# Kernel optimization log

Measured on AMD Instinct MI355X. Metric: run time of the kernel, lower is better.

The kernel has to match this reference:

```python
import jax, jax.numpy as jnp
import numpy as np

N = 20000
F_IN = 128
HID = 128
HEADS = 8
NCLS = 18
NEG_SLOPE = 0.2


def setup_inputs() -> dict:
    key = jax.random.key(0)
    ks = jax.random.split(key, 12)
    x = jax.random.normal(ks[0], (N, F_IN), dtype=jnp.float32)
    edge_index = jax.random.randint(ks[1], (2, 200000), 0, N)
    sc1 = 1.0 / np.sqrt(F_IN)
    sc2 = 1.0 / np.sqrt(HEADS * HID)
    W1 = jax.random.normal(ks[2], (F_IN, HEADS * HID), dtype=jnp.float32) * sc1
    a1_src = jax.random.normal(ks[3], (HEADS, HID), dtype=jnp.float32) * sc1
    a1_dst = jax.random.normal(ks[4], (HEADS, HID), dtype=jnp.float32) * sc1
    b1 = jnp.zeros((HEADS * HID,), dtype=jnp.float32)
    W2 = jax.random.normal(ks[5], (HEADS * HID, NCLS), dtype=jnp.float32) * sc2
    a2_src = jax.random.normal(ks[6], (1, NCLS), dtype=jnp.float32) * sc2
    a2_dst = jax.random.normal(ks[7], (1, NCLS), dtype=jnp.float32) * sc2
    b2 = jnp.zeros((NCLS,), dtype=jnp.float32)
    return {"x": x, "edge_index": edge_index, "W1": W1, "a1_src": a1_src,
            "a1_dst": a1_dst, "b1": b1, "W2": W2, "a2_src": a2_src,
            "a2_dst": a2_dst, "b2": b2}


def gat_conv(x, src, dst, W, a_src, a_dst, b, heads, out_ch):
    n = x.shape[0]
    h = (x @ W).reshape(n, heads, out_ch)              # [N,H,C]
    alpha_s = jnp.sum(h * a_src, axis=-1)              # [N,H]
    alpha_d = jnp.sum(h * a_dst, axis=-1)              # [N,H]
    e = jax.nn.leaky_relu(alpha_s[src] + alpha_d[dst], NEG_SLOPE)  # [E,H]
    # per-destination softmax (segment softmax)
    m = jax.ops.segment_max(e, dst, num_segments=n)
    e = jnp.exp(e - m[dst])
    z = jax.ops.segment_sum(e, dst, num_segments=n)
    alpha = e / (z[dst] + 1e-16)                       # [E,H]
    out = jax.ops.segment_sum(alpha[:, :, None] * h[src], dst, num_segments=n)
    return out.reshape(n, heads * out_ch) + b


def reference(x, edge_index, W1, a1_src, a1_dst, b1, W2, a2_src, a2_dst, b2):
    n = x.shape[0]
    # PyG GATConv adds self-loops by default
    loops = jnp.arange(n, dtype=edge_index.dtype)
    src = jnp.concatenate([edge_index[0], loops])
    dst = jnp.concatenate([edge_index[1], loops])
    h = gat_conv(x, src, dst, W1, a1_src, a1_dst, b1, HEADS, HID)
    h = jax.nn.relu(h)
    # F.dropout(training=self.training) is identity in eval mode
    out = gat_conv(h, src, dst, W2, a2_src, a2_dst, b2, 1, NCLS)
    return out
```

## Files before the change

kernel.cpp:

```cpp
#include <hip/hip_runtime.h>
#include <math.h>

#define FIN 128
#define NH 8
#define HC 128
#define HD (NH*HC)
#define NC 18
#define NW2 32
#define NEG 0.2f

typedef __attribute__((ext_vector_type(8))) short bf16x8;
typedef __attribute__((ext_vector_type(4))) float f32x4;

__device__ __forceinline__ float lrelu(float v){ return v > 0.f ? v : NEG*v; }

__device__ __forceinline__ unsigned short f2b(float f){
  unsigned u = __float_as_uint(f);
  unsigned r = (u + 0x7fffu + ((u >> 16) & 1u)) >> 16;
  return (unsigned short)r;
}
__device__ __forceinline__ float b2f_lo(unsigned u){ return __uint_as_float(u << 16); }
__device__ __forceinline__ float b2f_hi(unsigned u){ return __uint_as_float(u & 0xffff0000u); }

__device__ __forceinline__ void acc8(float* a, float w, uint4 r){
  a[0] += w*b2f_lo(r.x); a[1] += w*b2f_hi(r.x);
  a[2] += w*b2f_lo(r.y); a[3] += w*b2f_hi(r.y);
  a[4] += w*b2f_lo(r.z); a[5] += w*b2f_hi(r.z);
  a[6] += w*b2f_lo(r.w); a[7] += w*b2f_hi(r.w);
}

__global__ __launch_bounds__(1024) void scan_k(const int* __restrict__ deg, int N,
                                               int* __restrict__ off, int* __restrict__ cursor){
  __shared__ int wsum[16];
  int t = threadIdx.x, lane = t & 63, wid = t >> 6;
  int PER = (N + 1023) >> 10;
  int base = t * PER;
  int sum = 0;
  for (int i = 0; i < PER; ++i) {
    int idx = base + i;
    if (idx < N) sum += deg[idx];
  }
  int x = sum;
  #pragma unroll
  for (int o = 1; o < 64; o <<= 1) {
    int y = __shfl_up(x, o, 64);
    if (lane >= o) x += y;
  }
  if (lane == 63) wsum[wid] = x;
  __syncthreads();
  if (wid == 0 && lane < 16) {
    int wv = wsum[lane];
    #pragma unroll
    for (int o = 1; o < 16; o <<= 1) {
      int y = __shfl_up(wv, o, 16);
      if (lane >= o) wv += y;
    }
    wsum[lane] = wv;
  }
  __syncthreads();
  int carry = x - sum + (wid > 0 ? wsum[wid-1] : 0);
  int run = carry;
  for (int i = 0; i < PER; ++i) {
    int idx = base + i;
    if (idx < N) {
      off[idx] = run; cursor[idx] = run;
      run += deg[idx];
    }
  }
  if (base < N && base + PER >= N) off[N] = run;
}

__global__ void scatter_k(const int* __restrict__ ei, int E0, int N,
                          int* __restrict__ cursor, int* __restrict__ csr){
  int e = blockIdx.x*256 + threadIdx.x;
  int tot = E0 + N;
  if (e >= tot) return;
  int src, dst;
  if (e < E0) { src = ei[e]; dst = ei[E0 + e]; }
  else        { src = e - E0; dst = src; }
  int p = atomicAdd(&cursor[dst], 1);
  csr[p] = src;
}

__global__ __launch_bounds__(256) void prep_k(const float* __restrict__ x,
    const float* __restrict__ W1, const float* __restrict__ W2,
    const int* __restrict__ ei,
    unsigned short* __restrict__ xb, unsigned short* __restrict__ w1t,
    unsigned short* __restrict__ w2t, int* __restrict__ deg,
    int total8, int bX, int E0, int N){
  __shared__ unsigned short sT[FIN][64+2];
  int b = blockIdx.x, t = threadIdx.x;
  if (b < bX) {
    int i = b*256 + t;
    if (i < total8) {
      const float4* p = (const float4*)x + (size_t)i*2;
      float4 a = p[0], c = p[1];
      uint4 o;
      o.x = (unsigned)f2b(a.x) | ((unsigned)f2b(a.y) << 16);
      o.y = (unsigned)f2b(a.z) | ((unsigned)f2b(a.w) << 16);
      o.z = (unsigned)f2b(c.x) | ((unsigned)f2b(c.y) << 16);
      o.w = (unsigned)f2b(c.z) | ((unsigned)f2b(c.w) << 16);
      ((uint4*)xb)[i] = o;
    }
    return;
  }
  b -= bX;
  if (b < 16) {
    int n0 = b * 64;
    #pragma unroll
    for (int i = 0; i < 32; ++i) {
      int idx = i*256 + t;
      int k = idx >> 6, nl = idx & 63;
      sT[k][nl] = f2b(W1[(size_t)k*HD + n0 + nl]);
    }
    __syncthreads();
    #pragma unroll
    for (int i = 0; i < 16; ++i) {
      int nl = i*4 + (t >> 6);
      int kp = t & 63;
      unsigned u = (unsigned)sT[2*kp][nl] | ((unsigned)sT[2*kp+1][nl] << 16);
      *(unsigned*)&w1t[(size_t)(n0+nl)*FIN + 2*kp] = u;
    }
    return;
  }
  b -= 16;
  if (b < (NW2*HD)/256) {
    int idx = b*256 + t;
    int n = idx >> 10, k = idx & 1023;
    w2t[idx] = (n < NC) ? f2b(W2[(size_t)k*NC + n]) : (unsigned short)0;
    return;
  }
  b -= (NW2*HD)/256;
  {
    int e = b*256 + t;
    int tot = E0 + N;
    if (e >= tot) return;
    int dst = (e < E0) ? ei[E0 + e] : (e - E0);
    atomicAdd(&deg[dst], 1);
  }
}

__global__ __launch_bounds__(256) void gemm1_mfma_k(const unsigned short* __restrict__ xb,
    const unsigned short* __restrict__ w1t,
    const float* __restrict__ a1s, const float* __restrict__ a1d,
    unsigned short* __restrict__ g1b, float* __restrict__ as1, float* __restrict__ ad1,
    int N){
  __shared__ unsigned short sA[128][136];
  __shared__ unsigned short sB[128][136];
  __shared__ float sAs[2][128], sAd[2][128];
  int t = threadIdx.x, lane = t & 63, wid = t >> 6;
  int bm = blockIdx.x * 128;
  int head = blockIdx.y;
  int bn = head * 128;
  #pragma unroll
  for (int i = 0; i < 2; ++i) {
    int idx = i*256 + t;
    int row = idx >> 2, seg = idx & 3;
    int gm = bm + row;
    uint4 a0,a1,a2,a3;
    if (gm < N) {
      const uint4* gp = (const uint4*)(xb + (size_t)gm*FIN + seg*32);
      a0 = gp[0]; a1 = gp[1]; a2 = gp[2]; a3 = gp[3];
    } else {
      a0 = a1 = a2 = a3 = make_uint4(0,0,0,0);
    }
    uint4* lp = (uint4*)&sA[row][seg*32];
    lp[0]=a0; lp[1]=a1; lp[2]=a2; lp[3]=a3;
  }
  #pragma unroll
  for (int i = 0; i < 2; ++i) {
    int idx = i*256 + t;
    int row = idx >> 2, seg = idx & 3;
    const uint4* gp = (const uint4*)(w1t + (size_t)(bn + row)*FIN + seg*32);
    uint4* lp = (uint4*)&sB[row][seg*32];
    lp[0]=gp[0]; lp[1]=gp[1]; lp[2]=gp[2]; lp[3]=gp[3];
  }
  __syncthreads();
  int wr = wid >> 1, wc = wid & 1;
  int lr = lane & 15, kb = lane >> 4;
  f32x4 acc[4][4];
  #pragma unroll
  for (int mi = 0; mi < 4; ++mi)
    #pragma unroll
    for (int ni = 0; ni < 4; ++ni) {
      f32x4 z = {0.f, 0.f, 0.f, 0.f};
      acc[mi][ni] = z;
    }
  #pragma unroll
  for (int ks = 0; ks < 4; ++ks) {
    int ko = ks*32 + kb*8;
    bf16x8 a[4], b[4];
    #pragma unroll
    for (int mi = 0; mi < 4; ++mi)
      a[mi] = *(const bf16x8*)&sA[wr*64 + mi*16 + lr][ko];
    #pragma unroll
    for (int ni = 0; ni < 4; ++ni)
      b[ni] = *(const bf16x8*)&sB[wc*64 + ni*16 + lr][ko];
    #pragma unroll
    for (int mi = 0; mi < 4; ++mi)
      #pragma unroll
      for (int ni = 0; ni < 4; ++ni)
        acc[mi][ni] = __builtin_amdgcn_mfma_f32_16x16x32_bf16(a[mi], b[ni], acc[mi][ni], 0, 0, 0);
  }
  __syncthreads();

  float a1sv[4], a1dv[4];
  #pragma unroll
  for (int ni = 0; ni < 4; ++ni) {
    int c = wc*64 + ni*16 + lr;
    a1sv[ni] = a1s[head*HC + c];
    a1dv[ni] = a1d[head*HC + c];
  }
  #pragma unroll
  for (int mi = 0; mi < 4; ++mi) {
    #pragma unroll
    for (int r = 0; r < 4; ++r) {
      float ps = acc[mi][0][r]*a1sv[0] + acc[mi][1][r]*a1sv[1]
               + acc[mi][2][r]*a1sv[2] + acc[mi][3][r]*a1sv[3];
      float pd = acc[mi][0][r]*a1dv[0] + acc[mi][1][r]*a1dv[1]
               + acc[mi][2][r]*a1dv[2] + acc[mi][3][r]*a1dv[3];
      #pragma unroll
      for (int o = 1; o < 16; o <<= 1) {
        ps += __shfl_xor(ps, o, 64);
        pd += __shfl_xor(pd, o, 64);
      }
      if (lr == 0) {
        int row = wr*64 + mi*16 + kb*4 + r;
        sAs[wc][row] = ps;
        sAd[wc][row] = pd;
      }
    }
  }
  #pragma unroll
  for (int mi = 0; mi < 4; ++mi)
    #pragma unroll
    for (int ni = 0; ni < 4; ++ni) {
      int col = wc*64 + ni*16 + lr;
      #pragma unroll
      for (int r = 0; r < 4; ++r)
        sA[wr*64 + mi*16 + kb*4 + r][col] = f2b(acc[mi][ni][r]);
    }
  __syncthreads();
  {
    int row = t >> 1, half = t & 1;
    int grow = bm + row;
    if (grow < N) {
      uint4* dst = (uint4*)(g1b + (size_t)grow*HD + bn + half*64);
      const uint4* src = (const uint4*)&sA[row][half*64];
      #pragma unroll
      for (int q = 0; q < 8; ++q) dst[q] = src[q];
    }
    if (t < 128 && bm + t < N) {
      as1[(size_t)(bm + t)*NH + head] = sAs[0][t] + sAs[1][t];
      ad1[(size_t)(bm + t)*NH + head] = sAd[0][t] + sAd[1][t];
    }
  }
}

__global__ __launch_bounds__(256) void attn1_k(const unsigned short* __restrict__ g1b,
    const float* __restrict__ as1, const float* __restrict__ ad1,
    const int* __restrict__ off, const int* __restrict__ csr,
    const float* __restrict__ b1, unsigned short* __restrict__ hb, int N){
  int t = threadIdx.x, lane = t & 63, wid = t >> 6;
  int d = blockIdx.x*4 + wid;
  if (d >= N) return;
  int beg = off[d], deg = off[d+1] - beg;
  int hg = lane >> 3;
  float adg = ad1[d*NH + hg];
  float m = -1e30f, z = 0.f;
  float acc[16];
  #pragma unroll
  for (int i = 0; i < 16; ++i) acc[i] = 0.f;

  int j = 0;
  for (; j + 4 <= deg; j += 4) {
    int s0 = csr[beg+j+0], s1 = csr[beg+j+1], s2 = csr[beg+j+2], s3 = csr[beg+j+3];
    const uint4* p0 = (const uint4*)(g1b + (size_t)s0*HD) + lane*2;
    const uint4* p1 = (const uint4*)(g1b + (size_t)s1*HD) + lane*2;
    const uint4* p2 = (const uint4*)(g1b + (size_t)s2*HD) + lane*2;
    const uint4* p3 = (const uint4*)(g1b + (size_t)s3*HD) + lane*2;
    uint4 r00 = p0[0], r01 = p0[1];
    uint4 r10 = p1[0], r11 = p1[1];
    uint4 r20 = p2[0], r21 = p2[1];
    uint4 r30 = p3[0], r31 = p3[1];
    float e0 = lrelu(as1[s0*NH+hg] + adg);
    float e1 = lrelu(as1[s1*NH+hg] + adg);
    float e2 = lrelu(as1[s2*NH+hg] + adg);
    float e3 = lrelu(as1[s3*NH+hg] + adg);
    float em = fmaxf(fmaxf(e0,e1), fmaxf(e2,e3));
    if (em > m) {
      float sc = __expf(m - em);
      z *= sc;
      #pragma unroll
      for (int i = 0; i < 16; ++i) acc[i] *= sc;
      m = em;
    }
    float w0 = __expf(e0 - m), w1 = __expf(e1 - m);
    float w2 = __expf(e2 - m), w3 = __expf(e3 - m);
    z += w0 + w1 + w2 + w3;
    acc8(acc, w0, r00); acc8(acc+8, w0, r01);
    acc8(acc, w1, r10); acc8(acc+8, w1, r11);
    acc8(acc, w2, r20); acc8(acc+8, w2, r21);
    acc8(acc, w3, r30); acc8(acc+8, w3, r31);
  }
  for (; j < deg; ++j) {
    int s = csr[beg+j];
    const uint4* p = (const uint4*)(g1b + (size_t)s*HD) + lane*2;
    uint4 r0 = p[0], r1 = p[1];
    float e = lrelu(as1[s*NH+hg] + adg);
    if (e > m) {
      float sc = __expf(m - e);
      z *= sc;
      #pragma unroll
      for (int i = 0; i < 16; ++i) acc[i] *= sc;
      m = e;
    }
    float w = __expf(e - m);
    z += w;
    acc8(acc, w, r0); acc8(acc+8, w, r1);
  }

  float zinv = 1.f / (z + 1e-16f);
  int cb = lane*16;
  uint o[8];
  #pragma unroll
  for (int q = 0; q < 4; ++q) {
    float4 bv = *(const float4*)&b1[cb + q*4];
    float v0 = fmaxf(acc[q*4+0]*zinv + bv.x, 0.f);
    float v1 = fmaxf(acc[q*4+1]*zinv + bv.y, 0.f);
    float v2 = fmaxf(acc[q*4+2]*zinv + bv.z, 0.f);
    float v3 = fmaxf(acc[q*4+3]*zinv + bv.w, 0.f);
    o[q*2+0] = (unsigned)f2b(v0) | ((unsigned)f2b(v1) << 16);
    o[q*2+1] = (unsigned)f2b(v2) | ((unsigned)f2b(v3) << 16);
  }
  uint4* dst = (uint4*)(hb + (size_t)d*HD) + lane*2;
  dst[0] = make_uint4(o[0], o[1], o[2], o[3]);
  dst[1] = make_uint4(o[4], o[5], o[6], o[7]);
}

__global__ __launch_bounds__(256) void gemm2_k(const unsigned short* __restrict__ hb,
    const unsigned short* __restrict__ w2t, const float* __restrict__ a2s_g, const float* __restrict__ a2d_g,
    float* __restrict__ g2, float* __restrict__ as2, float* __restrict__ ad2, int N){
  __shared__ float red[4][32][32];
  int t = threadIdx.x, lane = t & 63, wid = t >> 6;
  int bm = blockIdx.x * 32;
  int lr = lane & 15, kb = lane >> 4;
  int kw = wid * 256;
  f32x4 acc[2][2];
  #pragma unroll
  for (int mi = 0; mi < 2; ++mi)
    #pragma unroll
    for (int ni = 0; ni < 2; ++ni) {
      f32x4 z = {0.f,0.f,0.f,0.f};
      acc[mi][ni] = z;
    }
  bf16x8 zf;
  #pragma unroll
  for (int q = 0; q < 8; ++q) zf[q] = 0;
  int r0n = bm + lr, r1n = bm + 16 + lr;
  #pragma unroll
  for (int ks = 0; ks < 8; ++ks) {
    int k = kw + ks*32 + kb*8;
    bf16x8 a0 = (r0n < N) ? *(const bf16x8*)&hb[(size_t)r0n*HD + k] : zf;
    bf16x8 a1 = (r1n < N) ? *(const bf16x8*)&hb[(size_t)r1n*HD + k] : zf;
    bf16x8 b0 = *(const bf16x8*)&w2t[(size_t)lr*HD + k];
    bf16x8 b1 = *(const bf16x8*)&w2t[(size_t)(16+lr)*HD + k];
    acc[0][0] = __builtin_amdgcn_mfma_f32_16x16x32_bf16(a0, b0, acc[0][0], 0,0,0);
    acc[0][1] = __builtin_amdgcn_mfma_f32_16x16x32_bf16(a0, b1, acc[0][1], 0,0,0);
    acc[1][0] = __builtin_amdgcn_mfma_f32_16x16x32_bf16(a1, b0, acc[1][0], 0,0,0);
    acc[1][1] = __builtin_amdgcn_mfma_f32_16x16x32_bf16(a1, b1, acc[1][1], 0,0,0);
  }
  #pragma unroll
  for (int mi = 0; mi < 2; ++mi)
    #pragma unroll
    for (int ni = 0; ni < 2; ++ni)
      #pragma unroll
      for (int r = 0; r < 4; ++r)
        red[wid][mi*16 + kb*4 + r][ni*16 + lr] = acc[mi][ni][r];
  __syncthreads();
  int row = t >> 3;
  int c4 = (t & 7) * 4;
  float tot[4];
  #pragma unroll
  for (int q = 0; q < 4; ++q)
    tot[q] = red[0][row][c4+q] + red[1][row][c4+q] + red[2][row][c4+q] + red[3][row][c4+q];
  int n = bm + row;
  float ps = 0.f, pd = 0.f;
  #pragma unroll
  for (int q = 0; q < 4; ++q) {
    int c = c4 + q;
    if (c < NC) {
      ps += tot[q]*a2s_g[c];
      pd += tot[q]*a2d_g[c];
    }
  }
  #pragma unroll
  for (int o = 1; o < 8; o <<= 1) {
    ps += __shfl_xor(ps, o, 8);
    pd += __shfl_xor(pd, o, 8);
  }
  if (n < N) {
    #pragma unroll
    for (int q = 0; q < 4; ++q) {
      int c = c4 + q;
      if (c < NC) g2[(size_t)n*NC + c] = tot[q];
    }
    if ((t & 7) == 0) { as2[n] = ps; ad2[n] = pd; }
  }
}

__global__ __launch_bounds__(256) void attn2_k(const float* __restrict__ g2,
    const float* __restrict__ as2, const float* __restrict__ ad2,
    const int* __restrict__ off, const int* __restrict__ csr,
    const float* __restrict__ b2, float* __restrict__ out, int N){
  int t = threadIdx.x, lane = t & 63, wid = t >> 6;
  int d = blockIdx.x*4 + wid;
  if (d >= N) return;
  int beg = off[d], deg = off[d+1] - beg;
  float adv = ad2[d];
  int g = lane / 18;
  int c = lane - g*18;
  float m = -1e30f, z = 0.f, acc = 0.f;
  if (g < 3) {
    int j = g;
    for (; j + 3 < deg; j += 6) {
      int sa = csr[beg+j], sb = csr[beg+j+3];
      float va = g2[(size_t)sa*NC + c];
      float vb = g2[(size_t)sb*NC + c];
      float ea = lrelu(as2[sa] + adv);
      float eb = lrelu(as2[sb] + adv);
      float em = fmaxf(ea, eb);
      if (em > m) { float sc = __expf(m - em); z *= sc; acc *= sc; m = em; }
      float wa = __expf(ea - m), wb = __expf(eb - m);
      z += wa + wb;
      acc += wa*va + wb*vb;
    }
    for (; j < deg; j += 3) {
      int s = csr[beg+j];
      float v = g2[(size_t)s*NC + c];
      float e = lrelu(as2[s] + adv);
      if (e > m) { float sc = __expf(m - e); z *= sc; acc *= sc; m = e; }
      float w = __expf(e - m);
      z += w;
      acc += w*v;
    }
  }
  float m0 = __shfl(m, 0),  m1 = __shfl(m, 18), m2 = __shfl(m, 36);
  float M  = fmaxf(m0, fmaxf(m1, m2));
  float e0 = __expf(m0 - M), e1 = __expf(m1 - M), e2 = __expf(m2 - M);
  float z0 = __shfl(z, 0),  z1 = __shfl(z, 18), z2 = __shfl(z, 36);
  int cl = (lane < NC) ? lane : 0;
  float a0 = __shfl(acc, cl), a1 = __shfl(acc, cl+18), a2 = __shfl(acc, cl+36);
  if (lane < NC) {
    float Z = z0*e0 + z1*e1 + z2*e2;
    float A = a0*e0 + a1*e1 + a2*e2;
    out[(size_t)d*NC + lane] = A / (Z + 1e-16f) + b2[lane];
  }
}

extern "C" void kernel_launch(void* const* d_in, const int* in_sizes, int n_in,
                              void* d_out, int out_size, void* d_ws, size_t ws_size,
                              hipStream_t stream){
  const float* x   = (const float*)d_in[0];
  const int*   ei  = (const int*)d_in[1];
  const float* W1  = (const float*)d_in[2];
  const float* a1s = (const float*)d_in[3];
  const float* a1d = (const float*)d_in[4];
  const float* b1  = (const float*)d_in[5];
  const float* W2  = (const float*)d_in[6];
  const float* a2s = (const float*)d_in[7];
  const float* a2d = (const float*)d_in[8];
  const float* b2  = (const float*)d_in[9];
  float* out = (float*)d_out;
  int N  = in_sizes[0] / FIN;
  int E0 = in_sizes[1] / 2;
  int Etot = E0 + N;

  float* as1 = (float*)d_ws;
  float* ad1 = as1 + (size_t)N*NH;
  float* g2  = ad1 + (size_t)N*NH;
  float* as2 = g2 + (size_t)N*NC;
  float* ad2 = as2 + N;
  unsigned short* g1b = (unsigned short*)(ad2 + N);
  unsigned short* hb  = g1b + (size_t)N*HD;
  int* deg    = (int*)(hb + (size_t)N*HD);
  int* off    = deg + N;
  int* cursor = off + N + 4;
  int* csr    = cursor + N;
  unsigned short* w2t = (unsigned short*)(csr + Etot);
  unsigned short* xb  = hb;
  unsigned short* w1t = hb + (size_t)N*FIN;

  hipMemsetAsync(deg, 0, sizeof(int)*(size_t)N, stream);

  int total8 = N*FIN/8;
  int bX = (total8 + 255)/256;
  int bH = (Etot + 255)/256;
  int bW2 = (NW2*HD)/256;
  prep_k<<<bX + 16 + bW2 + bH, 256, 0, stream>>>(x, W1, W2, ei, xb, w1t, w2t, deg,
                                                 total8, bX, E0, N);
  scan_k<<<1, 1024, 0, stream>>>(deg, N, off, cursor);
  scatter_k<<<(Etot+255)/256, 256, 0, stream>>>(ei, E0, N, cursor, csr);

  dim3 g1grid((N+127)/128, HD/128);
  gemm1_mfma_k<<<g1grid, 256, 0, stream>>>(xb, w1t, a1s, a1d, g1b, as1, ad1, N);
  attn1_k<<<(N+3)/4, 256, 0, stream>>>(g1b, as1, ad1, off, csr, b1, hb, N);
  gemm2_k<<<(N+31)/32, 256, 0, stream>>>(hb, w2t, a2s, a2d, g2, as2, ad2, N);
  attn2_k<<<(N+3)/4, 256, 0, stream>>>(g2, as2, ad2, off, csr, b2, out, N);
}
```

Measured before the change: 265.4 us.

## Fold attention vectors into W1 and split layer-1 aggregation across two waves

Precomputes W1·a_src and W1·a_dst per head as a 16x128 bf16 matrix in the prep kernel. The attention logits are then produced by one extra MFMA tile in the head-0 GEMM blocks, replacing the per-head shuffle reductions and shared-memory staging in the GEMM epilogue. The layer-1 aggregation kernel now uses two waves per destination node, each covering four heads with 8 channels per lane, and unrolls the edge loop by 8 instead of 4. This raises parallelism and memory-level parallelism, at the cost of reading the CSR indices twice and computing logits from bf16-rounded x and folded weights.

```diff
diff --git a/kernel.cpp b/kernel.cpp
--- a/kernel.cpp
+++ b/kernel.cpp
@@ -84,9 +84,11 @@
 
 __global__ __launch_bounds__(256) void prep_k(const float* __restrict__ x,
     const float* __restrict__ W1, const float* __restrict__ W2,
+    const float* __restrict__ a1s, const float* __restrict__ a1d,
     const int* __restrict__ ei,
     unsigned short* __restrict__ xb, unsigned short* __restrict__ w1t,
-    unsigned short* __restrict__ w2t, int* __restrict__ deg,
+    unsigned short* __restrict__ w2t, unsigned short* __restrict__ ut_g,
+    int* __restrict__ deg,
     int total8, int bX, int E0, int N){
   __shared__ unsigned short sT[FIN][64+2];
   int b = blockIdx.x, t = threadIdx.x;
@@ -131,6 +133,22 @@
     return;
   }
   b -= (NW2*HD)/256;
+  if (b < 1) {
+    #pragma unroll
+    for (int e8 = 0; e8 < 8; ++e8) {
+      int e = t*8 + e8;
+      int c = e >> 7, k = e & 127;
+      int h = c >> 1;
+      const float* av = (c & 1) ? &a1d[h*HC] : &a1s[h*HC];
+      const float* wr = &W1[(size_t)k*HD + h*HC];
+      float s = 0.f;
+      #pragma unroll 8
+      for (int cc = 0; cc < HC; ++cc) s += wr[cc]*av[cc];
+      ut_g[c*FIN + k] = f2b(s);
+    }
+    return;
+  }
+  b -= 1;
   {
     int e = b*256 + t;
     int tot = E0 + N;
@@ -141,13 +159,12 @@
 }
 
 __global__ __launch_bounds__(256) void gemm1_mfma_k(const unsigned short* __restrict__ xb,
-    const unsigned short* __restrict__ w1t,
-    const float* __restrict__ a1s, const float* __restrict__ a1d,
+    const unsigned short* __restrict__ w1t, const unsigned short* __restrict__ ut_g,
     unsigned short* __restrict__ g1b, float* __restrict__ as1, float* __restrict__ ad1,
     int N){
   __shared__ unsigned short sA[128][136];
   __shared__ unsigned short sB[128][136];
-  __shared__ float sAs[2][128], sAd[2][128];
+  __shared__ unsigned short sU[16][136];
   int t = threadIdx.x, lane = t & 63, wid = t >> 6;
   int bm = blockIdx.x * 128;
   int head = blockIdx.y;
@@ -175,17 +192,24 @@
     uint4* lp = (uint4*)&sB[row][seg*32];
     lp[0]=gp[0]; lp[1]=gp[1]; lp[2]=gp[2]; lp[3]=gp[3];
   }
+  bool alpha_blk = (head == 0);
+  if (alpha_blk) {
+    int row = t >> 4, seg = t & 15;
+    *(uint4*)&sU[row][seg*8] = *(const uint4*)&ut_g[row*FIN + seg*8];
+  }
   __syncthreads();
   int wr = wid >> 1, wc = wid & 1;
   int lr = lane & 15, kb = lane >> 4;
+  bool alpha_wave = alpha_blk && (wc == 0);
   f32x4 acc[4][4];
-  #pragma unroll
-  for (int mi = 0; mi < 4; ++mi)
-    #pragma unroll
-    for (int ni = 0; ni < 4; ++ni) {
-      f32x4 z = {0.f, 0.f, 0.f, 0.f};
-      acc[mi][ni] = z;
-    }
+  f32x4 accA[4];
+  #pragma unroll
+  for (int mi = 0; mi < 4; ++mi) {
+    f32x4 z = {0.f,0.f,0.f,0.f};
+    accA[mi] = z;
+    #pragma unroll
+    for (int ni = 0; ni < 4; ++ni) acc[mi][ni] = z;
+  }
   #pragma unroll
   for (int ks = 0; ks < 4; ++ks) {
     int ko = ks*32 + kb*8;
@@ -201,35 +225,25 @@
       #pragma unroll
       for (int ni = 0; ni < 4; ++ni)
         acc[mi][ni] = __builtin_amdgcn_mfma_f32_16x16x32_bf16(a[mi], b[ni], acc[mi][ni], 0, 0, 0);
+    if (alpha_wave) {
+      bf16x8 ub = *(const bf16x8*)&sU[lr][ko];
+      #pragma unroll
+      for (int mi = 0; mi < 4; ++mi)
+        accA[mi] = __builtin_amdgcn_mfma_f32_16x16x32_bf16(a[mi], ub, accA[mi], 0, 0, 0);
+    }
   }
   __syncthreads();
 
-  float a1sv[4], a1dv[4];
-  #pragma unroll
-  for (int ni = 0; ni < 4; ++ni) {
-    int c = wc*64 + ni*16 + lr;
-    a1sv[ni] = a1s[head*HC + c];
-    a1dv[ni] = a1d[head*HC + c];
-  }
-  #pragma unroll
-  for (int mi = 0; mi < 4; ++mi) {
-    #pragma unroll
-    for (int r = 0; r < 4; ++r) {
-      float ps = acc[mi][0][r]*a1sv[0] + acc[mi][1][r]*a1sv[1]
-               + acc[mi][2][r]*a1sv[2] + acc[mi][3][r]*a1sv[3];
-      float pd = acc[mi][0][r]*a1dv[0] + acc[mi][1][r]*a1dv[1]
-               + acc[mi][2][r]*a1dv[2] + acc[mi][3][r]*a1dv[3];
-      #pragma unroll
-      for (int o = 1; o < 16; o <<= 1) {
-        ps += __shfl_xor(ps, o, 64);
-        pd += __shfl_xor(pd, o, 64);
+  if (alpha_wave) {
+    int hcol = lr >> 1;
+    float* dst0 = (lr & 1) ? ad1 : as1;
+    #pragma unroll
+    for (int mi = 0; mi < 4; ++mi)
+      #pragma unroll
+      for (int r = 0; r < 4; ++r) {
+        int row = bm + wr*64 + mi*16 + kb*4 + r;
+        if (row < N) dst0[(size_t)row*NH + hcol] = accA[mi][r];
       }
-      if (lr == 0) {
-        int row = wr*64 + mi*16 + kb*4 + r;
-        sAs[wc][row] = ps;
-        sAd[wc][row] = pd;
-      }
-    }
   }
   #pragma unroll
   for (int mi = 0; mi < 4; ++mi)
@@ -250,10 +264,6 @@
       #pragma unroll
       for (int q = 0; q < 8; ++q) dst[q] = src[q];
     }
-    if (t < 128 && bm + t < N) {
-      as1[(size_t)(bm + t)*NH + head] = sAs[0][t] + sAs[1][t];
-      ad1[(size_t)(bm + t)*NH + head] = sAd[0][t] + sAd[1][t];
-    }
   }
 }
 
@@ -262,80 +272,79 @@
     const int* __restrict__ off, const int* __restrict__ csr,
     const float* __restrict__ b1, unsigned short* __restrict__ hb, int N){
   int t = threadIdx.x, lane = t & 63, wid = t >> 6;
-  int d = blockIdx.x*4 + wid;
+  int w = blockIdx.x*4 + wid;
+  int d = w >> 1, half = w & 1;
   if (d >= N) return;
   int beg = off[d], deg = off[d+1] - beg;
-  int hg = lane >> 3;
+  int hg = half*4 + (lane >> 4);
+  int cb = half*512 + lane*8;
   float adg = ad1[d*NH + hg];
   float m = -1e30f, z = 0.f;
-  float acc[16];
-  #pragma unroll
-  for (int i = 0; i < 16; ++i) acc[i] = 0.f;
+  float acc[8];
+  #pragma unroll
+  for (int i = 0; i < 8; ++i) acc[i] = 0.f;
 
   int j = 0;
-  for (; j + 4 <= deg; j += 4) {
-    int s0 = csr[beg+j+0], s1 = csr[beg+j+1], s2 = csr[beg+j+2], s3 = csr[beg+j+3];
-    const uint4* p0 = (const uint4*)(g1b + (size_t)s0*HD) + lane*2;
-    const uint4* p1 = (const uint4*)(g1b + (size_t)s1*HD) + lane*2;
-    const uint4* p2 = (const uint4*)(g1b + (size_t)s2*HD) + lane*2;
-    const uint4* p3 = (const uint4*)(g1b + (size_t)s3*HD) + lane*2;
-    uint4 r00 = p0[0], r01 = p0[1];
-    uint4 r10 = p1[0], r11 = p1[1];
-    uint4 r20 = p2[0], r21 = p2[1];
-    uint4 r30 = p3[0], r31 = p3[1];
-    float e0 = lrelu(as1[s0*NH+hg] + adg);
-    float e1 = lrelu(as1[s1*NH+hg] + adg);
-    float e2 = lrelu(as1[s2*NH+hg] + adg);
-    float e3 = lrelu(as1[s3*NH+hg] + adg);
-    float em = fmaxf(fmaxf(e0,e1), fmaxf(e2,e3));
+  for (; j + 8 <= deg; j += 8) {
+    int s[8];
+    #pragma unroll
+    for (int q = 0; q < 8; ++q) s[q] = csr[beg+j+q];
+    uint4 r[8];
+    #pragma unroll
+    for (int q = 0; q < 8; ++q) r[q] = *(const uint4*)(g1b + (size_t)s[q]*HD + cb);
+    float e[8];
+    #pragma unroll
+    for (int q = 0; q < 8; ++q) e[q] = lrelu(as1[s[q]*NH+hg] + adg);
+    float em = e[0];
+    #pragma unroll
+    for (int q = 1; q < 8; ++q) em = fmaxf(em, e[q]);
     if (em > m) {
       float sc = __expf(m - em);
       z *= sc;
       #pragma unroll
-      for (int i = 0; i < 16; ++i) acc[i] *= sc;
+      for (int i = 0; i < 8; ++i) acc[i] *= sc;
       m = em;
     }
-    float w0 = __expf(e0 - m), w1 = __expf(e1 - m);
-    float w2 = __expf(e2 - m), w3 = __expf(e3 - m);
-    z += w0 + w1 + w2 + w3;
-    acc8(acc, w0, r00); acc8(acc+8, w0, r01);
-    acc8(acc, w1, r10); acc8(acc+8, w1, r11);
-    acc8(acc, w2, r20); acc8(acc+8, w2, r21);
-    acc8(acc, w3, r30); acc8(acc+8, w3, r31);
+    #pragma unroll
+    for (int q = 0; q < 8; ++q) {
+      float wv = __expf(e[q] - m);
+      z += wv;
+      acc8(acc, wv, r[q]);
+    }
   }
   for (; j < deg; ++j) {
     int s = csr[beg+j];
-    const uint4* p = (const uint4*)(g1b + (size_t)s*HD) + lane*2;
-    uint4 r0 = p[0], r1 = p[1];
+    uint4 r = *(const uint4*)(g1b + (size_t)s*HD + cb);
     float e = lrelu(as1[s*NH+hg] + adg);
     if (e > m) {
       float sc = __expf(m - e);
       z *= sc;
       #pragma unroll
-      for (int i = 0; i < 16; ++i) acc[i] *= sc;
+      for (int i = 0; i < 8; ++i) acc[i] *= sc;
       m = e;
     }
-    float w = __expf(e - m);
-    z += w;
-    acc8(acc, w, r0); acc8(acc+8, w, r1);
+    float wv = __expf(e - m);
+    z += wv;
+    acc8(acc, wv, r);
   }
 
   float zinv = 1.f / (z + 1e-16f);
-  int cb = lane*16;
-  uint o[8];
-  #pragma unroll
-  for (int q = 0; q < 4; ++q) {
-    float4 bv = *(const float4*)&b1[cb + q*4];
-    float v0 = fmaxf(acc[q*4+0]*zinv + bv.x, 0.f);
-    float v1 = fmaxf(acc[q*4+1]*zinv + bv.y, 0.f);
-    float v2 = fmaxf(acc[q*4+2]*zinv + bv.z, 0.f);
-    float v3 = fmaxf(acc[q*4+3]*zinv + bv.w, 0.f);
-    o[q*2+0] = (unsigned)f2b(v0) | ((unsigned)f2b(v1) << 16);
-    o[q*2+1] = (unsigned)f2b(v2) | ((unsigned)f2b(v3) << 16);
-  }
-  uint4* dst = (uint4*)(hb + (size_t)d*HD) + lane*2;
-  dst[0] = make_uint4(o[0], o[1], o[2], o[3]);
-  dst[1] = make_uint4(o[4], o[5], o[6], o[7]);
+  float4 bv0 = *(const float4*)&b1[cb];
+  float4 bv1 = *(const float4*)&b1[cb+4];
+  float v0 = fmaxf(acc[0]*zinv + bv0.x, 0.f);
+  float v1 = fmaxf(acc[1]*zinv + bv0.y, 0.f);
+  float v2 = fmaxf(acc[2]*zinv + bv0.z, 0.f);
+  float v3 = fmaxf(acc[3]*zinv + bv0.w, 0.f);
+  float v4 = fmaxf(acc[4]*zinv + bv1.x, 0.f);
+  float v5 = fmaxf(acc[5]*zinv + bv1.y, 0.f);
+  float v6 = fmaxf(acc[6]*zinv + bv1.z, 0.f);
+  float v7 = fmaxf(acc[7]*zinv + bv1.w, 0.f);
+  uint4 o;
+  o.x = (unsigned)f2b(v0) | ((unsigned)f2b(v1) << 16);
+  o.y = (unsigned)f2b(v2) | ((unsigned)f2b(v3) << 16);
+  o.z = (unsigned)f2b(v4) | ((unsigned)f2b(v5) << 16);
+  o.w = (unsigned)f2b(v6) | ((unsigned)f2b(v7) << 16);
+  *(uint4*)(hb + (size_t)d*HD + cb) = o;
 }
 
 __global__ __launch_bounds__(256) void gemm2_k(const unsigned short* __restrict__ hb,
@@ -487,7 +496,8 @@
   int* off    = deg + N;
   int* cursor = off + N + 4;
   int* csr    = cursor + N;
-  unsigned short* w2t = (unsigned short*)(csr + Etot);
+  unsigned short* w2t  = (unsigned short*)(csr + Etot);
+  unsigned short* ut_g = w2t + (size_t)NW2*HD;
   unsigned short* xb  = hb;
   unsigned short* w1t = hb + (size_t)N*FIN;
 
@@ -497,14 +507,15 @@
   int bX = (total8 + 255)/256;
   int bH = (Etot + 255)/256;
   int bW2 = (NW2*HD)/256;
-  prep_k<<<bX + 16 + bW2 + bH, 256, 0, stream>>>(x, W1, W2, ei, xb, w1t, w2t, deg,
-                                                 total8, bX, E0, N);
+  prep_k<<<bX + 16 + bW2 + 1 + bH, 256, 0, stream>>>(x, W1, W2, a1s, a1d, ei,
+                                                     xb, w1t, w2t, ut_g, deg,
+                                                     total8, bX, E0, N);
   scan_k<<<1, 1024, 0, stream>>>(deg, N, off, cursor);
   scatter_k<<<(Etot+255)/256, 256, 0, stream>>>(ei, E0, N, cursor, csr);
 
   dim3 g1grid((N+127)/128, HD/128);
-  gemm1_mfma_k<<<g1grid, 256, 0, stream>>>(xb, w1t, a1s, a1d, g1b, as1, ad1, N);
-  attn1_k<<<(N+3)/4, 256, 0, stream>>>(g1b, as1, ad1, off, csr, b1, hb, N);
+  gemm1_mfma_k<<<g1grid, 256, 0, stream>>>(xb, w1t, ut_g, g1b, as1, ad1, N);
+  attn1_k<<<(2*N+3)/4, 256, 0, stream>>>(g1b, as1, ad1, off, csr, b1, hb, N);
   gemm2_k<<<(N+31)/32, 256, 0, stream>>>(hb, w2t, a2s, a2d, g2, as2, ad2, N);
   attn2_k<<<(N+3)/4, 256, 0, stream>>>(g2, as2, ad2, off, csr, b2, out, N);
 }
```

Measured after the change: 289.4 us. 1.09x slower.

## Fold attention vectors into W1 to compute alpha scores via extra MFMA

Applied to the files above, without the earlier changes.

Precomputes U = W1·a (per head, for source and destination) in the prep kernel and stores it as bf16. Only the head-0 blocks of the first GEMM run four extra MFMAs against U to produce all 16 alpha columns directly. This removes the per-head shuffle-reduction epilogue and its shared-memory staging from every block. The cost is extra bf16 rounding of U and of x·U, which changes the alpha values slightly compared with reducing the fp32 accumulators.

```diff
diff --git a/kernel.cpp b/kernel.cpp
--- a/kernel.cpp
+++ b/kernel.cpp
@@ -84,9 +84,11 @@
 
 __global__ __launch_bounds__(256) void prep_k(const float* __restrict__ x,
     const float* __restrict__ W1, const float* __restrict__ W2,
+    const float* __restrict__ a1s, const float* __restrict__ a1d,
     const int* __restrict__ ei,
     unsigned short* __restrict__ xb, unsigned short* __restrict__ w1t,
-    unsigned short* __restrict__ w2t, int* __restrict__ deg,
+    unsigned short* __restrict__ w2t, unsigned short* __restrict__ ut_g,
+    int* __restrict__ deg,
     int total8, int bX, int E0, int N){
   __shared__ unsigned short sT[FIN][64+2];
   int b = blockIdx.x, t = threadIdx.x;
@@ -131,6 +133,24 @@
     return;
   }
   b -= (NW2*HD)/256;
+  if (b < 16) {
+    int c = b;
+    int h = c >> 1;
+    const float* av = (c & 1) ? &a1d[h*HC] : &a1s[h*HC];
+    if (t < FIN) {
+      const float4* wr = (const float4*)&W1[(size_t)t*HD + h*HC];
+      const float4* ap = (const float4*)av;
+      float s = 0.f;
+      #pragma unroll 8
+      for (int q = 0; q < HC/4; ++q) {
+        float4 w4 = wr[q], a4 = ap[q];
+        s += w4.x*a4.x + w4.y*a4.y + w4.z*a4.z + w4.w*a4.w;
+      }
+      ut_g[c*FIN + t] = f2b(s);
+    }
+    return;
+  }
+  b -= 16;
   {
     int e = b*256 + t;
     int tot = E0 + N;
@@ -141,13 +161,12 @@
 }
 
 __global__ __launch_bounds__(256) void gemm1_mfma_k(const unsigned short* __restrict__ xb,
-    const unsigned short* __restrict__ w1t,
-    const float* __restrict__ a1s, const float* __restrict__ a1d,
+    const unsigned short* __restrict__ w1t, const unsigned short* __restrict__ ut_g,
     unsigned short* __restrict__ g1b, float* __restrict__ as1, float* __restrict__ ad1,
     int N){
   __shared__ unsigned short sA[128][136];
   __shared__ unsigned short sB[128][136];
-  __shared__ float sAs[2][128], sAd[2][128];
+  __shared__ unsigned short sU[16][136];
   int t = threadIdx.x, lane = t & 63, wid = t >> 6;
   int bm = blockIdx.x * 128;
   int head = blockIdx.y;
@@ -175,17 +194,24 @@
     uint4* lp = (uint4*)&sB[row][seg*32];
     lp[0]=gp[0]; lp[1]=gp[1]; lp[2]=gp[2]; lp[3]=gp[3];
   }
+  bool alpha_blk = (head == 0);
+  if (alpha_blk) {
+    int row = t >> 4, seg = t & 15;
+    *(uint4*)&sU[row][seg*8] = *(const uint4*)&ut_g[row*FIN + seg*8];
+  }
   __syncthreads();
   int wr = wid >> 1, wc = wid & 1;
   int lr = lane & 15, kb = lane >> 4;
+  bool alpha_wave = alpha_blk && (wc == 0);
   f32x4 acc[4][4];
-  #pragma unroll
-  for (int mi = 0; mi < 4; ++mi)
-    #pragma unroll
-    for (int ni = 0; ni < 4; ++ni) {
-      f32x4 z = {0.f, 0.f, 0.f, 0.f};
-      acc[mi][ni] = z;
-    }
+  f32x4 accA[4];
+  #pragma unroll
+  for (int mi = 0; mi < 4; ++mi) {
+    f32x4 z = {0.f,0.f,0.f,0.f};
+    accA[mi] = z;
+    #pragma unroll
+    for (int ni = 0; ni < 4; ++ni) acc[mi][ni] = z;
+  }
   #pragma unroll
   for (int ks = 0; ks < 4; ++ks) {
     int ko = ks*32 + kb*8;
@@ -201,35 +227,25 @@
       #pragma unroll
       for (int ni = 0; ni < 4; ++ni)
         acc[mi][ni] = __builtin_amdgcn_mfma_f32_16x16x32_bf16(a[mi], b[ni], acc[mi][ni], 0, 0, 0);
+    if (alpha_wave) {
+      bf16x8 ub = *(const bf16x8*)&sU[lr][ko];
+      #pragma unroll
+      for (int mi = 0; mi < 4; ++mi)
+        accA[mi] = __builtin_amdgcn_mfma_f32_16x16x32_bf16(a[mi], ub, accA[mi], 0, 0, 0);
+    }
   }
   __syncthreads();
 
-  float a1sv[4], a1dv[4];
-  #pragma unroll
-  for (int ni = 0; ni < 4; ++ni) {
-    int c = wc*64 + ni*16 + lr;
-    a1sv[ni] = a1s[head*HC + c];
-    a1dv[ni] = a1d[head*HC + c];
-  }
-  #pragma unroll
-  for (int mi = 0; mi < 4; ++mi) {
-    #pragma unroll
-    for (int r = 0; r < 4; ++r) {
-      float ps = acc[mi][0][r]*a1sv[0] + acc[mi][1][r]*a1sv[1]
-               + acc[mi][2][r]*a1sv[2] + acc[mi][3][r]*a1sv[3];
-      float pd = acc[mi][0][r]*a1dv[0] + acc[mi][1][r]*a1dv[1]
-               + acc[mi][2][r]*a1dv[2] + acc[mi][3][r]*a1dv[3];
-      #pragma unroll
-      for (int o = 1; o < 16; o <<= 1) {
-        ps += __shfl_xor(ps, o, 64);
-        pd += __shfl_xor(pd, o, 64);
+  if (alpha_wave) {
+    int hcol = lr >> 1;
+    float* dst0 = (lr & 1) ? ad1 : as1;
+    #pragma unroll
+    for (int mi = 0; mi < 4; ++mi)
+      #pragma unroll
+      for (int r = 0; r < 4; ++r) {
+        int row = bm + wr*64 + mi*16 + kb*4 + r;
+        if (row < N) dst0[(size_t)row*NH + hcol] = accA[mi][r];
       }
-      if (lr == 0) {
-        int row = wr*64 + mi*16 + kb*4 + r;
-        sAs[wc][row] = ps;
-        sAd[wc][row] = pd;
-      }
-    }
   }
   #pragma unroll
   for (int mi = 0; mi < 4; ++mi)
@@ -249,10 +265,6 @@
       const uint4* src = (const uint4*)&sA[row][half*64];
       #pragma unroll
       for (int q = 0; q < 8; ++q) dst[q] = src[q];
-    }
-    if (t < 128 && bm + t < N) {
-      as1[(size_t)(bm + t)*NH + head] = sAs[0][t] + sAs[1][t];
-      ad1[(size_t)(bm + t)*NH + head] = sAd[0][t] + sAd[1][t];
     }
   }
 }
@@ -487,7 +499,8 @@
   int* off    = deg + N;
   int* cursor = off + N + 4;
   int* csr    = cursor + N;
-  unsigned short* w2t = (unsigned short*)(csr + Etot);
+  unsigned short* w2t  = (unsigned short*)(csr + Etot);
+  unsigned short* ut_g = w2t + (size_t)NW2*HD;
   unsigned short* xb  = hb;
   unsigned short* w1t = hb + (size_t)N*FIN;
 
@@ -497,13 +510,14 @@
   int bX = (total8 + 255)/256;
   int bH = (Etot + 255)/256;
   int bW2 = (NW2*HD)/256;
-  prep_k<<<bX + 16 + bW2 + bH, 256, 0, stream>>>(x, W1, W2, ei, xb, w1t, w2t, deg,
-                                                 total8, bX, E0, N);
+  prep_k<<<bX + 16 + bW2 + 16 + bH, 256, 0, stream>>>(x, W1, W2, a1s, a1d, ei,
+                                                      xb, w1t, w2t, ut_g, deg,
+                                                      total8, bX, E0, N);
   scan_k<<<1, 1024, 0, stream>>>(deg, N, off, cursor);
   scatter_k<<<(Etot+255)/256, 256, 0, stream>>>(ei, E0, N, cursor, csr);
 
   dim3 g1grid((N+127)/128, HD/128);
-  gemm1_mfma_k<<<g1grid, 256, 0, stream>>>(xb, w1t, a1s, a1d, g1b, as1, ad1, N);
+  gemm1_mfma_k<<<g1grid, 256, 0, stream>>>(xb, w1t, ut_g, g1b, as1, ad1, N);
   attn1_k<<<(N+3)/4, 256, 0, stream>>>(g1b, as1, ad1, off, csr, b1, hb, N);
   gemm2_k<<<(N+31)/32, 256, 0, stream>>>(hb, w2t, a2s, a2d, g2, as2, ad2, N);
   attn2_k<<<(N+3)/4, 256, 0, stream>>>(g2, as2, ad2, off, csr, b2, out, N);
```

Measured after the change: 255.1 us. 3.9% less time.
